# Performance work log

Hardware: AMD Instinct MI355X
Metric: run time of the kernel (lower is better)

The kernel has to match this reference:

```python
import jax, jax.numpy as jnp
import numpy as np

H, DH = 8, 40                      # heads, dim_head
SCALE = DH ** -0.5
NEG = -3.4028235e38                # -finfo(float32).max
EMBDIM, STEPS, EMBEDS = 512, 1000, 50


def _gelu(x):
    return jax.nn.gelu(x, approximate=False)  # torch.nn.GELU default (erf)


def setup_inputs() -> dict:
    key = jax.random.key(0)
    ks = jax.random.split(key, 16)
    b, i, j = 16, 4096, 77
    qd, cd, inner = 320, 768, 320
    s = lambda k, sh, f: jax.random.normal(k, sh, jnp.float32) * f
    bc2 = jnp.tile(jnp.array([0.0, -3.0], jnp.float32), H)  # INITBIAS on class 1
    return dict(
        x=jax.random.normal(ks[0], (b, i, qd), jnp.float32),
        embs=jax.random.normal(ks[1], (b, j, cd), jnp.float32),
        cam=jax.random.uniform(ks[2], (b, i, j), jnp.float32),
        progress=jax.random.uniform(ks[3], (b,), jnp.float32),
        strength=jnp.float32(1.0),
        Wq=s(ks[4], (qd, inner), qd ** -0.5),
        Wk=s(ks[5], (cd, inner), cd ** -0.5),
        Wv=s(ks[6], (cd, inner), cd ** -0.5),
        Wo=s(ks[7], (inner, qd), inner ** -0.5),
        bo=jnp.zeros((qd,), jnp.float32),
        emb1=s(ks[8], (EMBEDS + 1, EMBDIM), 1.0),
        emb2=s(ks[9], (STEPS // EMBEDS, EMBDIM), 1.0),
        Wc1=s(ks[10], (EMBDIM, EMBDIM), EMBDIM ** -0.5),
        bc1=jnp.zeros((EMBDIM,), jnp.float32),
        Wc2=s(ks[11], (EMBDIM, 2 * H), EMBDIM ** -0.5),
        bc2=bc2,
        captiontypes=jax.random.randint(ks[12], (b, j), 0, 5),
    )


def reference(x, embs, cam, progress, strength, Wq, Wk, Wv, Wo, bo,
              emb1, emb2, Wc1, bc1, Wc2, bc2, captiontypes):
    b, i, _ = x.shape
    j = embs.shape[1]
    # projections, split heads: 'b n (h d) -> (b h) n d'
    q = (x @ Wq).reshape(b, i, H, DH).transpose(0, 2, 1, 3).reshape(b * H, i, DH)
    k = (embs @ Wk).reshape(b, j, H, DH).transpose(0, 2, 1, 3).reshape(b * H, j, DH)
    v = (embs @ Wv).reshape(b, j, H, DH).transpose(0, 2, 1, 3).reshape(b * H, j, DH)
    # fp32 QK^T (fp32 already)
    sim = jnp.einsum('bid,bjd->bij', q.astype(jnp.float32), k.astype(jnp.float32))

    # cross_attention_control (CustomCrossAttentionMinimal)
    mask2 = jnp.repeat((captiontypes >= 2)[:, None, :], H, axis=0)  # [(bh),1,j]
    # weight_func under no_grad: std of sim where captiontypes>=2 (unbiased)
    sim_sg = jax.lax.stop_gradient(sim)
    mfull = jnp.broadcast_to(mask2, sim.shape)
    n = mfull.sum().astype(jnp.float32)
    mean = jnp.sum(jnp.where(mfull, sim_sg, 0.0)) / n
    var = jnp.sum(jnp.where(mfull, (sim_sg - mean) ** 2, 0.0)) / (n - 1.0)
    simstd = jnp.sqrt(var)
    wf = jax.lax.stop_gradient(cam * simstd * strength)        # [b,i,j]
    wf = jnp.repeat(wf[:, None], H, axis=1).reshape(b * H, i, j)
    wf = jnp.where(mask2, wf, 0.0)
    useglobal = wf.sum(-1) == 0                                 # [(bh),i]
    wfmax = wf.max(-1, keepdims=True)
    wfb = wf >= (jnp.maximum(wfmax, 0.001) - 0.0001)            # bool [(bh),i,j]
    gmask = jnp.repeat(((captiontypes >= 0) & (captiontypes < 2))[:, None, :], H, axis=0)
    lmask = wfb | (useglobal[:, :, None] & gmask)
    gattn = jax.nn.softmax(jnp.where(gmask, sim, NEG) * SCALE, axis=-1)
    lattn = jax.nn.softmax(jnp.where(lmask, sim, NEG) * SCALE, axis=-1)

    # ProgressClassifier: DiscretizedProgressEmbed -> GELU -> Linear -> GELU -> Linear
    xstep = jnp.minimum(jnp.round(progress * STEPS).astype(jnp.int32), STEPS - 1)
    per = STEPS // EMBEDS  # 20
    e = emb1[xstep // per] + emb2[xstep % per]                  # [b, 512]
    e = _gelu(_gelu(e) @ Wc1 + bc1)
    logits = e @ Wc2 + bc2                                      # [b, 2H]
    pc = jax.nn.softmax(logits.reshape(b, H, 2), axis=-1).reshape(b * H, 2)

    attn = gattn * pc[:, 0, None, None] + lattn * pc[:, 1, None, None]
    out = jnp.einsum('bij,bjd->bid', attn, v.astype(jnp.float32))
    out = out.reshape(b, H, i, DH).transpose(0, 2, 1, 3).reshape(b, i, H * DH)
    return out @ Wo + bo
```

## Files before the change

kernel.cpp:

```cpp
#include <hip/hip_runtime.h>


typedef _Float16 vh8 __attribute__((ext_vector_type(8)));
typedef _Float16 vh4 __attribute__((ext_vector_type(4)));
typedef float    vf4 __attribute__((ext_vector_type(4)));

#define NEGBIG  (-3.4028235e38f)
#define SC2     (0.15811388300841897f * 1.4426950408889634f)
#define INFF    (__builtin_inff())

__device__ __forceinline__ vh8 h8zero() {
  vh8 v;
#pragma unroll
  for (int i = 0; i < 8; ++i) v[i] = (_Float16)0.f;
  return v;
}
__device__ __forceinline__ vf4 f4zero() {
  vf4 v;
#pragma unroll
  for (int i = 0; i < 4; ++i) v[i] = 0.f;
  return v;
}
__device__ __forceinline__ float gelu_exact(float x) {
  return 0.5f * x * (1.0f + erff(x * 0.70710678118654752f));
}
__device__ __forceinline__ unsigned swzA(int row) {
  return (unsigned)(((row & 7) << 4) ^ (((row >> 3) & 1) << 5));
}
__device__ __forceinline__ unsigned swzB(int row) {
  return (unsigned)((row & 7) << 4);
}
__device__ __forceinline__ void glds16(const void* g, void* l) {
  __builtin_amdgcn_global_load_lds((const __attribute__((address_space(1))) unsigned*)g,
                                   (__attribute__((address_space(3))) unsigned*)l, 16, 0, 0);
}

__global__ __launch_bounds__(256) void transpose_kernel(
    const float* __restrict__ Wq, const float* __restrict__ Wk,
    const float* __restrict__ Wv, const float* __restrict__ Wo,
    _Float16* __restrict__ WqT, _Float16* __restrict__ WkvT, _Float16* __restrict__ WoT)
{
  __shared__ float ts[32][33];
  int tile = blockIdx.x;
  const float* src; _Float16* dst; int dstK, rowOff;
  if (tile < 100)      { src = Wq; dst = WqT;  dstK = 320; rowOff = 0; }
  else if (tile < 340) { src = Wk; dst = WkvT; dstK = 768; rowOff = 0;   tile -= 100; }
  else if (tile < 580) { src = Wv; dst = WkvT; dstK = 768; rowOff = 320; tile -= 340; }
  else                 { src = Wo; dst = WoT;  dstK = 320; rowOff = 0;   tile -= 580; }
  int kb = tile / 10, nb = tile - kb * 10;
  int k0 = kb * 32, n0 = nb * 32;
  int r = threadIdx.x >> 5, c = threadIdx.x & 31;
#pragma unroll
  for (int p = 0; p < 4; ++p)
    ts[r + p * 8][c] = src[(size_t)(k0 + r + p * 8) * 320 + n0 + c];
  __syncthreads();
#pragma unroll
  for (int p = 0; p < 4; ++p)
    dst[(size_t)(rowOff + n0 + r + p * 8) * dstK + k0 + c] = (_Float16)ts[c][r + p * 8];
}

__global__ __launch_bounds__(256) void vtrans_kernel(
    const _Float16* __restrict__ vf, unsigned* __restrict__ vTg32)
{
  const int b = blockIdx.x, h = blockIdx.y, t = threadIdx.x;
  unsigned* out = vTg32 + (size_t)(b * 8 + h) * 3072;
#pragma unroll
  for (int p = 0; p < 12; ++p) {
    int idx = t + p * 256;
    int d = idx >> 6;
    int u = idx & 63;
    int c = u >> 2, pr = u & 3;
    int sd = (int)(swzA(d) >> 4);
    int j0 = ((c ^ sd) << 3) + pr * 2;
    unsigned lo = 0, hi = 0;
    if (d < 40) {
      if (j0 < 77)     lo = *(const unsigned short*)(vf + (size_t)(b * 77 + j0) * 640 + h * 40 + d);
      if (j0 + 1 < 77) hi = *(const unsigned short*)(vf + (size_t)(b * 77 + j0 + 1) * 640 + h * 40 + d);
    }
    out[idx] = lo | (hi << 16);
  }
}

__global__ __launch_bounds__(256) void kv_gemm_kernel(
    const float* __restrict__ Ap, const _Float16* __restrict__ Bt,
    _Float16* __restrict__ Cp)
{
  const int t = threadIdx.x, lane = t & 63, wave = t >> 6;
  const int m0 = blockIdx.x * 64;
  const int n0 = blockIdx.y * 160;
  const int l15 = lane & 15, l4 = lane >> 4;
  const int rg = wave >> 1, cg = wave & 1;

  vf4 acc[2][5];
#pragma unroll
  for (int a = 0; a < 2; ++a)
#pragma unroll
    for (int bq = 0; bq < 5; ++bq) acc[a][bq] = f4zero();

#pragma unroll 2
  for (int kk = 0; kk < 24; ++kk) {
    int k = kk * 32 + l4 * 8;
    vh8 av[2];
#pragma unroll
    for (int mt = 0; mt < 2; ++mt) {
      int row = m0 + rg * 32 + mt * 16 + l15;
      av[mt] = h8zero();
      if (row < 1232) {
        const float* ap = Ap + (size_t)row * 768 + k;
        float4 f0 = *(const float4*)ap;
        float4 f1 = *(const float4*)(ap + 4);
        vh8 hv;
        hv[0] = (_Float16)f0.x; hv[1] = (_Float16)f0.y; hv[2] = (_Float16)f0.z; hv[3] = (_Float16)f0.w;
        hv[4] = (_Float16)f1.x; hv[5] = (_Float16)f1.y; hv[6] = (_Float16)f1.z; hv[7] = (_Float16)f1.w;
        av[mt] = hv;
      }
    }
#pragma unroll
    for (int nt = 0; nt < 5; ++nt) {
      int n = n0 + cg * 80 + nt * 16 + l15;
      vh8 bv = *(const vh8*)(Bt + (size_t)n * 768 + k);
      acc[0][nt] = __builtin_amdgcn_mfma_f32_16x16x32_f16(av[0], bv, acc[0][nt], 0, 0, 0);
      acc[1][nt] = __builtin_amdgcn_mfma_f32_16x16x32_f16(av[1], bv, acc[1][nt], 0, 0, 0);
    }
  }
#pragma unroll
  for (int mt = 0; mt < 2; ++mt)
#pragma unroll
    for (int nt = 0; nt < 5; ++nt) {
      int n = n0 + cg * 80 + nt * 16 + l15;
#pragma unroll
      for (int r = 0; r < 4; ++r) {
        int m = m0 + rg * 32 + mt * 16 + l4 * 4 + r;
        if (m < 1232) Cp[(size_t)m * 640 + n] = (_Float16)acc[mt][nt][r];
      }
    }
}

__global__ __launch_bounds__(256) void qproj_kernel(
    const float* __restrict__ x, const _Float16* __restrict__ Bt,
    _Float16* __restrict__ qhm)
{
  __shared__ __align__(16) char smem[40960];
  _Float16* Bs = (_Float16*)smem;
  const int t = threadIdx.x, lane = t & 63, wave = t >> 6;
  const int m0 = blockIdx.x * 64;
  const int l15 = lane & 15, l4 = lane >> 4;
  const int wbase = t & ~63;
  const int rg = wave >> 1, cg = wave & 1;
  const float* arow0 = x + (size_t)(m0 + rg * 32 + l15) * 320 + l4 * 8;
  const float* arow1 = x + (size_t)(m0 + rg * 32 + 16 + l15) * 320 + l4 * 8;

  vf4 acc[2][10];
#pragma unroll
  for (int a = 0; a < 2; ++a)
#pragma unroll
    for (int bq = 0; bq < 10; ++bq) acc[a][bq] = f4zero();

  float4 fA[8], fB[8];
#pragma unroll
  for (int ks = 0; ks < 2; ++ks) {
    fA[ks * 4 + 0] = *(const float4*)(arow0 + ks * 32);
    fA[ks * 4 + 1] = *(const float4*)(arow0 + ks * 32 + 4);
    fA[ks * 4 + 2] = *(const float4*)(arow1 + ks * 32);
    fA[ks * 4 + 3] = *(const float4*)(arow1 + ks * 32 + 4);
  }

#pragma unroll
  for (int kc = 0; kc < 5; ++kc) {
    int k0 = kc * 64;
    __syncthreads();
#pragma unroll
    for (int p = 0; p < 10; ++p) {
      int idx = t + p * 256;
      int n = idx >> 3, c8 = idx & 7;
      glds16(Bt + (size_t)n * 320 + k0 + ((c8 ^ (n & 7)) << 3),
             (char*)Bs + (size_t)(p * 256 + wbase) * 16);
    }
    float4* nxt = (kc & 1) ? fA : fB;
    if (kc < 4) {
      int k0n = k0 + 64;
#pragma unroll
      for (int ks = 0; ks < 2; ++ks) {
        nxt[ks * 4 + 0] = *(const float4*)(arow0 + k0n + ks * 32);
        nxt[ks * 4 + 1] = *(const float4*)(arow0 + k0n + ks * 32 + 4);
        nxt[ks * 4 + 2] = *(const float4*)(arow1 + k0n + ks * 32);
        nxt[ks * 4 + 3] = *(const float4*)(arow1 + k0n + ks * 32 + 4);
      }
    }
    __syncthreads();
    float4* cur = (kc & 1) ? fB : fA;
#pragma unroll
    for (int ks = 0; ks < 2; ++ks) {
      vh8 av[2];
#pragma unroll
      for (int mt = 0; mt < 2; ++mt) {
        float4 f0 = cur[ks * 4 + mt * 2 + 0];
        float4 f1 = cur[ks * 4 + mt * 2 + 1];
        vh8 hv;
        hv[0] = (_Float16)f0.x; hv[1] = (_Float16)f0.y; hv[2] = (_Float16)f0.z; hv[3] = (_Float16)f0.w;
        hv[4] = (_Float16)f1.x; hv[5] = (_Float16)f1.y; hv[6] = (_Float16)f1.z; hv[7] = (_Float16)f1.w;
        av[mt] = hv;
      }
#pragma unroll
      for (int nt = 0; nt < 10; ++nt) {
        int n = cg * 160 + nt * 16 + l15;
        unsigned byte = (unsigned)(n * 128 + (ks * 32 + l4 * 8) * 2) ^ swzB(n);
        vh8 bv = *(const vh8*)((const char*)Bs + byte);
        acc[0][nt] = __builtin_amdgcn_mfma_f32_16x16x32_f16(av[0], bv, acc[0][nt], 0, 0, 0);
        acc[1][nt] = __builtin_amdgcn_mfma_f32_16x16x32_f16(av[1], bv, acc[1][nt], 0, 0, 0);
      }
    }
  }

  __syncthreads();
#pragma unroll
  for (int mt = 0; mt < 2; ++mt)
#pragma unroll
    for (int nt = 0; nt < 10; ++nt) {
      int col = cg * 160 + nt * 16 + l15;
#pragma unroll
      for (int r = 0; r < 4; ++r) {
        int lr = rg * 32 + mt * 16 + l4 * 4 + r;
        unsigned byte = (unsigned)(lr * 640 + col * 2) ^ swzB(lr);
        *(_Float16*)(smem + byte) = (_Float16)acc[mt][nt][r];
      }
    }
  __syncthreads();
#pragma unroll
  for (int p = 0; p < 10; ++p) {
    int idx = t + p * 256;
    int h = idx / 320;
    int rem = idx - h * 320;
    int lrow = rem / 5;
    int c = rem - lrow * 5;
    unsigned sb = (unsigned)(lrow * 640 + h * 80 + c * 16) ^ swzB(lrow);
    vh8 v = *(const vh8*)(smem + sb);
    int gi = m0 + lrow;
    int bb = gi >> 12, ii = gi & 4095;
    *(vh8*)(qhm + ((size_t)(bb * 8 + h) * 4096 + ii) * 40 + c * 8) = v;
  }
}

__global__ __launch_bounds__(256) void oproj_kernel(
    const _Float16* __restrict__ hohm, const _Float16* __restrict__ Bt,
    const float* __restrict__ bias, float* __restrict__ out)
{
  __shared__ __align__(16) _Float16 Bs[320 * 64];
  const int t = threadIdx.x, lane = t & 63, wave = t >> 6;
  const int m0 = blockIdx.x * 64;
  const int l15 = lane & 15, l4 = lane >> 4;
  const int wbase = t & ~63;
  const int rg = wave >> 1, cg = wave & 1;

  const int gi0 = m0 + rg * 32 + l15;
  const int gi1 = gi0 + 16;
  const int bb0 = gi0 >> 12, ii0 = gi0 & 4095;
  const int bb1 = gi1 >> 12, ii1 = gi1 & 4095;

  vf4 acc[2][10];
#pragma unroll
  for (int a = 0; a < 2; ++a)
#pragma unroll
    for (int bq = 0; bq < 10; ++bq) acc[a][bq] = f4zero();

  auto aload = [&](int k) -> vh8 { return h8zero(); };

  vh8 hA[4], hB[4];
#pragma unroll
  for (int ks = 0; ks < 2; ++ks) {
    int k = ks * 32 + l4 * 8;
    int hh = k / 40, d = k - hh * 40;
    hA[ks * 2 + 0] = *(const vh8*)(hohm + ((size_t)(bb0 * 8 + hh) * 4096 + ii0) * 40 + d);
    hA[ks * 2 + 1] = *(const vh8*)(hohm + ((size_t)(bb1 * 8 + hh) * 4096 + ii1) * 40 + d);
  }

#pragma unroll
  for (int kc = 0; kc < 5; ++kc) {
    int k0 = kc * 64;
    __syncthreads();
#pragma unroll
    for (int p = 0; p < 10; ++p) {
      int idx = t + p * 256;
      int n = idx >> 3, c8 = idx & 7;
      glds16(Bt + (size_t)n * 320 + k0 + ((c8 ^ (n & 7)) << 3),
             (char*)Bs + (size_t)(p * 256 + wbase) * 16);
    }
    vh8* nxt = (kc & 1) ? hA : hB;
    if (kc < 4) {
#pragma unroll
      for (int ks = 0; ks < 2; ++ks) {
        int k = k0 + 64 + ks * 32 + l4 * 8;
        int hh = k / 40, d = k - hh * 40;
        nxt[ks * 2 + 0] = *(const vh8*)(hohm + ((size_t)(bb0 * 8 + hh) * 4096 + ii0) * 40 + d);
        nxt[ks * 2 + 1] = *(const vh8*)(hohm + ((size_t)(bb1 * 8 + hh) * 4096 + ii1) * 40 + d);
      }
    }
    __syncthreads();
    vh8* cur = (kc & 1) ? hB : hA;
#pragma unroll
    for (int ks = 0; ks < 2; ++ks) {
#pragma unroll
      for (int nt = 0; nt < 10; ++nt) {
        int n = cg * 160 + nt * 16 + l15;
        unsigned byte = (unsigned)(n * 128 + (ks * 32 + l4 * 8) * 2) ^ swzB(n);
        vh8 bv = *(const vh8*)((const char*)Bs + byte);
        acc[0][nt] = __builtin_amdgcn_mfma_f32_16x16x32_f16(cur[ks * 2 + 0], bv, acc[0][nt], 0, 0, 0);
        acc[1][nt] = __builtin_amdgcn_mfma_f32_16x16x32_f16(cur[ks * 2 + 1], bv, acc[1][nt], 0, 0, 0);
      }
    }
  }
#pragma unroll
  for (int mt = 0; mt < 2; ++mt)
#pragma unroll
    for (int nt = 0; nt < 10; ++nt) {
      int n = cg * 160 + nt * 16 + l15;
      float bias_v = bias[n];
#pragma unroll
      for (int r = 0; r < 4; ++r) {
        int m = m0 + rg * 32 + mt * 16 + l4 * 4 + r;
        out[(size_t)m * 320 + n] = acc[mt][nt][r] + bias_v;
      }
    }
}

__global__ __launch_bounds__(256) void classifier_kernel(
    const float* __restrict__ progress,
    const float* __restrict__ emb1, const float* __restrict__ emb2,
    const float* __restrict__ Wc1, const float* __restrict__ bc1,
    const float* __restrict__ Wc2, const float* __restrict__ bc2,
    float* __restrict__ pcb)
{
  __shared__ float g[512];
  __shared__ float h1[512];
  __shared__ float lg[16];
  const int b = blockIdx.x;
  const int t = threadIdx.x;

  float pr = progress[b];
  int xstep = (int)rintf(pr * 1000.0f);
  if (xstep > 999) xstep = 999;
  int a = xstep / 20;
  int r = xstep - a * 20;

  for (int d = t; d < 512; d += 256) {
    float e = emb1[a * 512 + d] + emb2[r * 512 + d];
    g[d] = gelu_exact(e);
  }
  __syncthreads();
  for (int n = t; n < 512; n += 256) {
    float acc = bc1[n];
    for (int d = 0; d < 512; ++d) acc = fmaf(g[d], Wc1[d * 512 + n], acc);
    h1[n] = gelu_exact(acc);
  }
  __syncthreads();
  if (t < 16) {
    float acc = bc2[t];
    for (int d = 0; d < 512; ++d) acc = fmaf(h1[d], Wc2[d * 16 + t], acc);
    lg[t] = acc;
  }
  __syncthreads();
  if (t < 8) {
    float a0 = lg[2 * t], a1 = lg[2 * t + 1];
    float mx = fmaxf(a0, a1);
    float e0 = __expf(a0 - mx), e1 = __expf(a1 - mx);
    float inv = 1.0f / (e0 + e1);
    pcb[(b * 8 + t) * 2 + 0] = e0 * inv;
    pcb[(b * 8 + t) * 2 + 1] = e1 * inv;
  }
}

__global__ __launch_bounds__(256) void std_kernel(
    const _Float16* __restrict__ qhm, const _Float16* __restrict__ kf,
    const int* __restrict__ ctypes, double* __restrict__ partials)
{
  __shared__ __align__(16) _Float16 qt[64 * 40];
  const int t = threadIdx.x, lane = t & 63, wave = t >> 6;
  const int it = blockIdx.x, b = blockIdx.y, h = blockIdx.z;
  const int i0 = it * 64;
  const int l15 = lane & 15, l4 = lane >> 4;

  const _Float16* qsrc = qhm + ((size_t)(b * 8 + h) * 4096 + i0) * 40;
  glds16(qsrc + t * 8, (char*)qt + t * 16);
  if (t < 64) glds16(qsrc + (256 + t) * 8, (char*)qt + (256 + t) * 16);
  __syncthreads();

  int qrow = wave * 16 + l15;
  vh8 a0 = *(const vh8*)((const char*)qt + qrow * 80 + l4 * 16);
  vh8 a1 = h8zero();
  if (l4 == 0) a1 = *(const vh8*)((const char*)qt + qrow * 80 + 64);

  double S = 0.0, S2 = 0.0;
#pragma unroll
  for (int jt = 0; jt < 5; ++jt) {
    int j = jt * 16 + l15;
    bool valid = (j < 77);
    vh8 b0 = h8zero(), b1 = h8zero();
    int ctj = -1;
    if (valid) {
      const _Float16* kp = kf + (size_t)(b * 77 + j) * 640 + h * 40;
      b0 = *(const vh8*)(kp + l4 * 8);
      if (l4 == 0) b1 = *(const vh8*)(kp + 32);
      ctj = ctypes[b * 77 + j];
    }
    vf4 s = f4zero();
    s = __builtin_amdgcn_mfma_f32_16x16x32_f16(a0, b0, s, 0, 0, 0);
    s = __builtin_amdgcn_mfma_f32_16x16x32_f16(a1, b1, s, 0, 0, 0);
    if (ctj >= 2) {
#pragma unroll
      for (int r = 0; r < 4; ++r) {
        double sv = (double)s[r];
        S += sv; S2 += sv * sv;
      }
    }
  }
#pragma unroll
  for (int off = 32; off > 0; off >>= 1) {
    S += __shfl_xor(S, off);
    S2 += __shfl_xor(S2, off);
  }
  if (lane == 0) {
    int idx = (((b * 64 + it) * 8) + h) * 4 + wave;
    partials[2 * idx + 0] = S;
    partials[2 * idx + 1] = S2;
  }
}

__global__ __launch_bounds__(256) void finalize_kernel(
    const double* __restrict__ partials, const int* __restrict__ ctypes,
    float* __restrict__ ssb)
{
  __shared__ double rs[256];
  __shared__ double rs2[256];
  __shared__ int rc[256];
  const int t = threadIdx.x;
  double S = 0.0, S2 = 0.0;
#pragma unroll
  for (int p = 0; p < 128; ++p) {
    int idx = t + p * 256;
    S += partials[2 * idx + 0];
    S2 += partials[2 * idx + 1];
  }
  int c = 0;
#pragma unroll
  for (int p = 0; p < 5; ++p) {
    int idx = t + p * 256;
    if (idx < 1232) c += (ctypes[idx] >= 2) ? 1 : 0;
  }
  rs[t] = S; rs2[t] = S2; rc[t] = c;
  __syncthreads();
  for (int off = 128; off > 0; off >>= 1) {
    if (t < off) { rs[t] += rs[t + off]; rs2[t] += rs2[t + off]; rc[t] += rc[t + off]; }
    __syncthreads();
  }
  if (t == 0) {
    double n = (double)rc[0] * 8.0 * 4096.0;
    double mean = rs[0] / n;
    double var = (rs2[0] - n * mean * mean) / (n - 1.0);
    ssb[0] = (float)sqrt(var > 0.0 ? var : 0.0);
  }
}

__global__ __launch_bounds__(256) void lmask_kernel(
    const float* __restrict__ cam, const int* __restrict__ ctypes,
    const float* __restrict__ ssb, const float* __restrict__ strengthp,
    unsigned* __restrict__ lmp)
{
  __shared__ float camt[64 * 81];
  __shared__ unsigned char gmv[96];
  __shared__ unsigned char m2v[96];
  const int t = threadIdx.x;
  const int it = blockIdx.x, b = blockIdx.y;
  const int i0 = it * 64;

  if (t < 96) {
    int j = t;
    int ct = (j < 77) ? ctypes[b * 77 + j] : -1;
    gmv[j] = (j < 77 && ct >= 0 && ct < 2) ? 1 : 0;
    m2v[j] = (j < 77 && ct >= 2) ? 1 : 0;
  }
#pragma unroll
  for (int p = 0; p < 20; ++p) {
    int idx = t + p * 256;
    int row = idx / 80;
    int j = idx - row * 80;
    camt[row * 81 + j] = (j < 77) ? cam[((size_t)b * 4096 + i0 + row) * 77 + j] : 0.f;
  }
  __syncthreads();

  const float ss = ssb[0];
  const float st = strengthp[0];
  int row = t >> 2, qd = t & 3;
  float wfv[20];
  float wmax = 0.f, wsum = 0.f;
#pragma unroll
  for (int m = 0; m < 20; ++m) {
    int j = qd + 4 * m;
    float wf = 0.f;
    if (j < 77 && m2v[j]) wf = (camt[row * 81 + j] * ss) * st;
    wfv[m] = wf;
    wmax = fmaxf(wmax, wf);
    wsum += wf;
  }
  wmax = fmaxf(wmax, __shfl_xor(wmax, 1));
  wmax = fmaxf(wmax, __shfl_xor(wmax, 2));
  wsum += __shfl_xor(wsum, 1);
  wsum += __shfl_xor(wsum, 2);
  float thr = fmaxf(wmax, 0.001f) - 0.0001f;
  bool ug = (wsum == 0.f);
  unsigned wbits = 0u;
#pragma unroll
  for (int m = 0; m < 20; ++m) {
    int j = qd + 4 * m;
    bool lv = (wfv[m] >= thr) || (ug && (j < 77) && gmv[j]);
    if (lv) wbits |= (1u << m);
  }
  lmp[((size_t)b * 4096 + i0 + row) * 4 + qd] = wbits;
}

__global__ __launch_bounds__(256) void attn_kernel(
    const _Float16* __restrict__ qhm, const _Float16* __restrict__ kf,
    const unsigned* __restrict__ vTg32, const int* __restrict__ ctypes,
    const float* __restrict__ pcb, const unsigned* __restrict__ lmp,
    _Float16* __restrict__ hohm)
{
  __shared__ _Float16 vT[48 * 128];
  __shared__ _Float16 attnbuf[64 * 128];
  __shared__ __align__(16) _Float16 qt[64 * 40];
  __shared__ unsigned lmw[256];
  __shared__ float gbf[96];
  __shared__ float nbf[96];

  const int t = threadIdx.x, lane = t & 63, wave = t >> 6;
  const int it = blockIdx.x, b = blockIdx.y, h = blockIdx.z;
  const int i0 = it * 64;
  const int l15 = lane & 15, l4 = lane >> 4;

  if (t < 96) {
    int j = t;
    bool valid = (j < 77);
    int ct = valid ? ctypes[b * 77 + j] : -1;
    bool gm = valid && ct >= 0 && ct < 2;
    gbf[j] = gm ? 0.f : (valid ? NEGBIG : -INFF);
    nbf[j] = valid ? NEGBIG : -INFF;
  }
  lmw[t] = lmp[((size_t)b * 4096 + i0) * 4 + t];

  const _Float16* qsrc = qhm + ((size_t)(b * 8 + h) * 4096 + i0) * 40;
  glds16(qsrc + t * 8, (char*)qt + t * 16);
  if (t < 64) glds16(qsrc + (256 + t) * 8, (char*)qt + (256 + t) * 16);

  {
    const unsigned* src0 = vTg32 + (size_t)(b * 8 + h) * 3072;
#pragma unroll
    for (int p = 0; p < 3; ++p) {
      int idx = t + p * 256;
      glds16(src0 + idx * 4, (char*)vT + (size_t)(p * 256 + (t & ~63)) * 16);
    }
  }
#pragma unroll
  for (int p = 0; p < 2; ++p) {
    int idx = t + p * 256;
    int row = idx >> 3, c = idx & 7;
    unsigned byte = (unsigned)(row * 256 + 160 + c * 4) ^ swzA(row);
    *(unsigned*)((char*)attnbuf + byte) = 0u;
  }

  vh8 k0v[5], k1v[5];
#pragma unroll
  for (int jt = 0; jt < 5; ++jt) {
    int j = jt * 16 + l15;
    k0v[jt] = h8zero(); k1v[jt] = h8zero();
    if (j < 77) {
      const _Float16* kp = kf + (size_t)(b * 77 + j) * 640 + h * 40;
      k0v[jt] = *(const vh8*)(kp + l4 * 8);
      if (l4 == 0) k1v[jt] = *(const vh8*)(kp + 32);
    }
  }

  __syncthreads();

  const int myrow = wave * 16 + l15;
  vh8 qf0 = *(const vh8*)((const char*)qt + myrow * 80 + l4 * 16);
  vh8 qf1 = h8zero();
  if (l4 == 0) qf1 = *(const vh8*)((const char*)qt + myrow * 80 + 64);

  vf4 sacc[5];
#pragma unroll
  for (int jt = 0; jt < 5; ++jt) sacc[jt] = f4zero();
#pragma unroll
  for (int jt = 0; jt < 5; ++jt) {
    sacc[jt] = __builtin_amdgcn_mfma_f32_16x16x32_f16(k0v[jt], qf0, sacc[jt], 0, 0, 0);
    sacc[jt] = __builtin_amdgcn_mfma_f32_16x16x32_f16(k1v[jt], qf1, sacc[jt], 0, 0, 0);
  }

  const float pc0 = pcb[(b * 8 + h) * 2 + 0];
  const float pc1 = pcb[(b * 8 + h) * 2 + 1];
  unsigned wbits[4];
#pragma unroll
  for (int r = 0; r < 4; ++r) wbits[r] = lmw[myrow * 4 + r];

  float gv[5][4], lv[5][4];
  float mg = -INFF, ml = -INFF;
#pragma unroll
  for (int jt = 0; jt < 5; ++jt) {
    int jbase = jt * 16 + l4 * 4;
    float4 gb4 = *(const float4*)&gbf[jbase];
    float4 nb4 = *(const float4*)&nbf[jbase];
    const float* gbp = (const float*)&gb4;
    const float* nbp = (const float*)&nb4;
#pragma unroll
    for (int r = 0; r < 4; ++r) {
      float sv = sacc[jt][r];
      float g = fmaf(sv, SC2, gbp[r]);
      unsigned bit = (wbits[r] >> (jt * 4 + l4)) & 1u;
      float l = fmaf(sv, SC2, bit ? 0.f : nbp[r]);
      gv[jt][r] = g; lv[jt][r] = l;
      mg = fmaxf(mg, g); ml = fmaxf(ml, l);
    }
  }
  mg = fmaxf(mg, __shfl_xor(mg, 16)); mg = fmaxf(mg, __shfl_xor(mg, 32));
  ml = fmaxf(ml, __shfl_xor(ml, 16)); ml = fmaxf(ml, __shfl_xor(ml, 32));
  float sG = 0.f, sL = 0.f;
#pragma unroll
  for (int jt = 0; jt < 5; ++jt)
#pragma unroll
    for (int r = 0; r < 4; ++r) {
      float eg = exp2f(gv[jt][r] - mg);
      float el = exp2f(lv[jt][r] - ml);
      gv[jt][r] = eg; lv[jt][r] = el;
      sG += eg; sL += el;
    }
  sG += __shfl_xor(sG, 16); sG += __shfl_xor(sG, 32);
  sL += __shfl_xor(sL, 16); sL += __shfl_xor(sL, 32);
  float rG = pc0 / sG, rL = pc1 / sL;
  {
    unsigned swz = swzA(myrow);
    unsigned rowbase = (unsigned)(myrow * 256);
#pragma unroll
    for (int jt = 0; jt < 5; ++jt) {
      vh4 w;
#pragma unroll
      for (int r = 0; r < 4; ++r)
        w[r] = (_Float16)fmaf(gv[jt][r], rG, lv[jt][r] * rL);
      unsigned byte = (rowbase + (unsigned)((jt * 16 + l4 * 4) * 2)) ^ swz;
      *(vh4*)((char*)attnbuf + byte) = w;
    }
  }
  __syncthreads();

  vf4 oacc[3];
#pragma unroll
  for (int nt = 0; nt < 3; ++nt) oacc[nt] = f4zero();
#pragma unroll
  for (int ks = 0; ks < 3; ++ks) {
    int arow = wave * 16 + l15;
    unsigned abyte = (unsigned)(arow * 256 + (ks * 32 + l4 * 8) * 2) ^ swzA(arow);
    vh8 pa = *(const vh8*)((const char*)attnbuf + abyte);
#pragma unroll
    for (int nt = 0; nt < 3; ++nt) {
      int n = nt * 16 + l15;
      unsigned byte = (unsigned)(n * 256 + (ks * 32 + l4 * 8) * 2) ^ swzA(n);
      vh8 vb = *(const vh8*)((const char*)vT + byte);
      oacc[nt] = __builtin_amdgcn_mfma_f32_16x16x32_f16(pa, vb, oacc[nt], 0, 0, 0);
    }
  }
#pragma unroll
  for (int nt = 0; nt < 3; ++nt) {
    int d = nt * 16 + l15;
    if (d < 40) {
#pragma unroll
      for (int r = 0; r < 4; ++r) {
        int m = wave * 16 + l4 * 4 + r;
        qt[m * 40 + d] = (_Float16)oacc[nt][r];
      }
    }
  }
  __syncthreads();

  _Float16* obase = hohm + ((size_t)(b * 8 + h) * 4096 + i0) * 40;
  {
    vh8 v = *(const vh8*)((const char*)qt + t * 16);
    *(vh8*)(obase + t * 8) = v;
  }
  if (t < 64) {
    vh8 v = *(const vh8*)((const char*)qt + (256 + t) * 16);
    *(vh8*)(obase + (256 + t) * 8) = v;
  }
}

extern "C" void kernel_launch(void* const* d_in, const int* in_sizes, int n_in,
                              void* d_out, int out_size, void* d_ws, size_t ws_size,
                              hipStream_t stream)
{
  const float* x        = (const float*)d_in[0];
  const float* embs     = (const float*)d_in[1];
  const float* cam      = (const float*)d_in[2];
  const float* progress = (const float*)d_in[3];
  const float* strength = (const float*)d_in[4];
  const float* Wq       = (const float*)d_in[5];
  const float* Wk       = (const float*)d_in[6];
  const float* Wv       = (const float*)d_in[7];
  const float* Wo       = (const float*)d_in[8];
  const float* bo       = (const float*)d_in[9];
  const float* emb1     = (const float*)d_in[10];
  const float* emb2     = (const float*)d_in[11];
  const float* Wc1      = (const float*)d_in[12];
  const float* bc1      = (const float*)d_in[13];
  const float* Wc2      = (const float*)d_in[14];
  const float* bc2      = (const float*)d_in[15];
  const int*   ctypes   = (const int*)d_in[16];

  char* w = (char*)d_ws;
  auto alloc = [&](size_t bytes) { char* p = w; w += (bytes + 255) & ~(size_t)255; return p; };
  _Float16* qhm   = (_Float16*)alloc(65536ull * 320 * 2);
  _Float16* hohm  = (_Float16*)alloc(65536ull * 320 * 2);
  _Float16* kvb   = (_Float16*)alloc(1232ull * 640 * 2);
  unsigned* vTg   = (unsigned*)alloc(128ull * 3072 * 4);
  _Float16* WqT   = (_Float16*)alloc(320ull * 320 * 2);
  _Float16* WkvT  = (_Float16*)alloc(640ull * 768 * 2);
  _Float16* WoT   = (_Float16*)alloc(320ull * 320 * 2);
  unsigned* lmp   = (unsigned*)alloc(65536ull * 4 * 4);
  float*    pcb   = (float*)alloc(256 * 4);
  double*   part  = (double*)alloc(32768ull * 2 * 8);
  float*    ssb   = (float*)alloc(256);

  transpose_kernel<<<680, 256, 0, stream>>>(Wq, Wk, Wv, Wo, WqT, WkvT, WoT);
  classifier_kernel<<<16, 256, 0, stream>>>(progress, emb1, emb2, Wc1, bc1, Wc2, bc2, pcb);
  kv_gemm_kernel<<<dim3(20, 4), 256, 0, stream>>>(embs, WkvT, kvb);
  vtrans_kernel<<<dim3(16, 8), 256, 0, stream>>>(kvb + 320, vTg);
  qproj_kernel<<<1024, 256, 0, stream>>>(x, WqT, qhm);
  std_kernel<<<dim3(64, 16, 8), 256, 0, stream>>>(qhm, kvb, ctypes, part);
  finalize_kernel<<<1, 256, 0, stream>>>(part, ctypes, ssb);
  lmask_kernel<<<dim3(64, 16), 256, 0, stream>>>(cam, ctypes, ssb, strength, lmp);
  attn_kernel<<<dim3(64, 16, 8), 256, 0, stream>>>(qhm, kvb, vTg, ctypes, pcb, lmp, hohm);
  oproj_kernel<<<1024, 256, 0, stream>>>(hohm, WoT, bo, (float*)d_out);
}
```

Measured before the change: 283.2 us.

## Fuse std partial-sum computation into qproj kernel and drop std_kernel

Computes the masked sim sum and sum-of-squares partials inside qproj_kernel, reusing the Q tile already staged in shared memory, instead of re-reading qhm in a separate std_kernel launch. Partials shrink to one per wave of each qproj block, and finalize reads fewer entries. The softmax exponent also switches from exp2f with a log2e-folded scale to __expf with the plain scale. This adds register pressure and an epilogue tail to the qproj kernel.

```diff
diff --git a/kernel.cpp b/kernel.cpp
--- a/kernel.cpp
+++ b/kernel.cpp
@@ -6,7 +6,7 @@
 typedef float    vf4 __attribute__((ext_vector_type(4)));
 
 #define NEGBIG  (-3.4028235e38f)
-#define SC2     (0.15811388300841897f * 1.4426950408889634f)
+#define SCALE_F 0.15811388300841897f
 #define INFF    (__builtin_inff())
 
 __device__ __forceinline__ vh8 h8zero() {
@@ -138,7 +138,8 @@
 
 __global__ __launch_bounds__(256) void qproj_kernel(
     const float* __restrict__ x, const _Float16* __restrict__ Bt,
-    _Float16* __restrict__ qhm)
+    const _Float16* __restrict__ kf, const int* __restrict__ ctypes,
+    _Float16* __restrict__ qhm, double* __restrict__ partials)
 {
   __shared__ __align__(16) char smem[40960];
   _Float16* Bs = (_Float16*)smem;
@@ -239,6 +240,63 @@
     int bb = gi >> 12, ii = gi & 4095;
     *(vh8*)(qhm + ((size_t)(bb * 8 + h) * 4096 + ii) * 40 + c * 8) = v;
   }
+
+  {
+    const int b = m0 >> 12;
+    double S = 0.0, S2 = 0.0;
+#pragma unroll
+    for (int ho = 0; ho < 2; ++ho) {
+      int h = wave * 2 + ho;
+      vh8 a0v[4], a1v[4];
+#pragma unroll
+      for (int mt = 0; mt < 4; ++mt) {
+        int qrow = mt * 16 + l15;
+        unsigned b0 = (unsigned)(qrow * 640 + (h * 40 + l4 * 8) * 2) ^ swzB(qrow);
+        a0v[mt] = *(const vh8*)(smem + b0);
+        a1v[mt] = h8zero();
+        if (l4 == 0) {
+          unsigned b1 = (unsigned)(qrow * 640 + (h * 40 + 32) * 2) ^ swzB(qrow);
+          a1v[mt] = *(const vh8*)(smem + b1);
+        }
+      }
+#pragma unroll
+      for (int jt = 0; jt < 5; ++jt) {
+        int j = jt * 16 + l15;
+        bool valid = (j < 77);
+        vh8 b0 = h8zero(), b1 = h8zero();
+        int ctj = -1;
+        if (valid) {
+          const _Float16* kp = kf + (size_t)(b * 77 + j) * 640 + h * 40;
+          b0 = *(const vh8*)(kp + l4 * 8);
+          if (l4 == 0) b1 = *(const vh8*)(kp + 32);
+          ctj = ctypes[b * 77 + j];
+        }
+#pragma unroll
+        for (int mt = 0; mt < 4; ++mt) {
+          vf4 s = f4zero();
+          s = __builtin_amdgcn_mfma_f32_16x16x32_f16(a0v[mt], b0, s, 0, 0, 0);
+          s = __builtin_amdgcn_mfma_f32_16x16x32_f16(a1v[mt], b1, s, 0, 0, 0);
+          if (ctj >= 2) {
+#pragma unroll
+            for (int r = 0; r < 4; ++r) {
+              double sv = (double)s[r];
+              S += sv; S2 += sv * sv;
+            }
+          }
+        }
+      }
+    }
+#pragma unroll
+    for (int off = 32; off > 0; off >>= 1) {
+      S += __shfl_xor(S, off);
+      S2 += __shfl_xor(S2, off);
+    }
+    if (lane == 0) {
+      int idx = blockIdx.x * 4 + wave;
+      partials[2 * idx + 0] = S;
+      partials[2 * idx + 1] = S2;
+    }
+  }
 }
 
 __global__ __launch_bounds__(256) void oproj_kernel(
@@ -262,8 +320,6 @@
   for (int a = 0; a < 2; ++a)
 #pragma unroll
     for (int bq = 0; bq < 10; ++bq) acc[a][bq] = f4zero();
-
-  auto aload = [&](int k) -> vh8 { return h8zero(); };
 
   vh8 hA[4], hB[4];
 #pragma unroll
@@ -369,62 +425,6 @@
   }
 }
 
-__global__ __launch_bounds__(256) void std_kernel(
-    const _Float16* __restrict__ qhm, const _Float16* __restrict__ kf,
-    const int* __restrict__ ctypes, double* __restrict__ partials)
-{
-  __shared__ __align__(16) _Float16 qt[64 * 40];
-  const int t = threadIdx.x, lane = t & 63, wave = t >> 6;
-  const int it = blockIdx.x, b = blockIdx.y, h = blockIdx.z;
-  const int i0 = it * 64;
-  const int l15 = lane & 15, l4 = lane >> 4;
-
-  const _Float16* qsrc = qhm + ((size_t)(b * 8 + h) * 4096 + i0) * 40;
-  glds16(qsrc + t * 8, (char*)qt + t * 16);
-  if (t < 64) glds16(qsrc + (256 + t) * 8, (char*)qt + (256 + t) * 16);
-  __syncthreads();
-
-  int qrow = wave * 16 + l15;
-  vh8 a0 = *(const vh8*)((const char*)qt + qrow * 80 + l4 * 16);
-  vh8 a1 = h8zero();
-  if (l4 == 0) a1 = *(const vh8*)((const char*)qt + qrow * 80 + 64);
-
-  double S = 0.0, S2 = 0.0;
-#pragma unroll
-  for (int jt = 0; jt < 5; ++jt) {
-    int j = jt * 16 + l15;
-    bool valid = (j < 77);
-    vh8 b0 = h8zero(), b1 = h8zero();
-    int ctj = -1;
-    if (valid) {
-      const _Float16* kp = kf + (size_t)(b * 77 + j) * 640 + h * 40;
-      b0 = *(const vh8*)(kp + l4 * 8);
-      if (l4 == 0) b1 = *(const vh8*)(kp + 32);
-      ctj = ctypes[b * 77 + j];
-    }
-    vf4 s = f4zero();
-    s = __builtin_amdgcn_mfma_f32_16x16x32_f16(a0, b0, s, 0, 0, 0);
-    s = __builtin_amdgcn_mfma_f32_16x16x32_f16(a1, b1, s, 0, 0, 0);
-    if (ctj >= 2) {
-#pragma unroll
-      for (int r = 0; r < 4; ++r) {
-        double sv = (double)s[r];
-        S += sv; S2 += sv * sv;
-      }
-    }
-  }
-#pragma unroll
-  for (int off = 32; off > 0; off >>= 1) {
-    S += __shfl_xor(S, off);
-    S2 += __shfl_xor(S2, off);
-  }
-  if (lane == 0) {
-    int idx = (((b * 64 + it) * 8) + h) * 4 + wave;
-    partials[2 * idx + 0] = S;
-    partials[2 * idx + 1] = S2;
-  }
-}
-
 __global__ __launch_bounds__(256) void finalize_kernel(
     const double* __restrict__ partials, const int* __restrict__ ctypes,
     float* __restrict__ ssb)
@@ -435,7 +435,7 @@
   const int t = threadIdx.x;
   double S = 0.0, S2 = 0.0;
 #pragma unroll
-  for (int p = 0; p < 128; ++p) {
+  for (int p = 0; p < 16; ++p) {
     int idx = t + p * 256;
     S += partials[2 * idx + 0];
     S2 += partials[2 * idx + 1];
@@ -611,9 +611,9 @@
 #pragma unroll
     for (int r = 0; r < 4; ++r) {
       float sv = sacc[jt][r];
-      float g = fmaf(sv, SC2, gbp[r]);
+      float g = fmaf(sv, SCALE_F, gbp[r]);
       unsigned bit = (wbits[r] >> (jt * 4 + l4)) & 1u;
-      float l = fmaf(sv, SC2, bit ? 0.f : nbp[r]);
+      float l = fmaf(sv, SCALE_F, bit ? 0.f : nbp[r]);
       gv[jt][r] = g; lv[jt][r] = l;
       mg = fmaxf(mg, g); ml = fmaxf(ml, l);
     }
@@ -625,8 +625,8 @@
   for (int jt = 0; jt < 5; ++jt)
 #pragma unroll
     for (int r = 0; r < 4; ++r) {
-      float eg = exp2f(gv[jt][r] - mg);
-      float el = exp2f(lv[jt][r] - ml);
+      float eg = __expf(gv[jt][r] - mg);
+      float el = __expf(lv[jt][r] - ml);
       gv[jt][r] = eg; lv[jt][r] = el;
       sG += eg; sL += el;
     }
@@ -721,15 +721,14 @@
   _Float16* WoT   = (_Float16*)alloc(320ull * 320 * 2);
   unsigned* lmp   = (unsigned*)alloc(65536ull * 4 * 4);
   float*    pcb   = (float*)alloc(256 * 4);
-  double*   part  = (double*)alloc(32768ull * 2 * 8);
+  double*   part  = (double*)alloc(4096ull * 2 * 8);
   float*    ssb   = (float*)alloc(256);
 
   transpose_kernel<<<680, 256, 0, stream>>>(Wq, Wk, Wv, Wo, WqT, WkvT, WoT);
   classifier_kernel<<<16, 256, 0, stream>>>(progress, emb1, emb2, Wc1, bc1, Wc2, bc2, pcb);
   kv_gemm_kernel<<<dim3(20, 4), 256, 0, stream>>>(embs, WkvT, kvb);
   vtrans_kernel<<<dim3(16, 8), 256, 0, stream>>>(kvb + 320, vTg);
-  qproj_kernel<<<1024, 256, 0, stream>>>(x, WqT, qhm);
-  std_kernel<<<dim3(64, 16, 8), 256, 0, stream>>>(qhm, kvb, ctypes, part);
+  qproj_kernel<<<1024, 256, 0, stream>>>(x, WqT, kvb, ctypes, qhm, part);
   finalize_kernel<<<1, 256, 0, stream>>>(part, ctypes, ssb);
   lmask_kernel<<<dim3(64, 16), 256, 0, stream>>>(cam, ctypes, ssb, strength, lmp);
   attn_kernel<<<dim3(64, 16, 8), 256, 0, stream>>>(qhm, kvb, vTg, ctypes, pcb, lmp, hohm);
```

New measurement: 253.4 us. -10.5%, faster.
